# Kernel tuning notes

Hardware: AMD Instinct MI355X
Metric: run time of the kernel (lower is better)

The kernel has to match this reference:

```python
import jax, jax.numpy as jnp
import numpy as np

B, T, F = 256, 288, 64
UNITS = [128, 64, 64, 32]
SCALE = 0.05  # small init so relu-activated recurrence stays numerically stable


def _lstm_scan(x_tbf, Wk, Wr, b):
    """Keras LSTM with activation=relu, recurrent_activation=sigmoid.
    x_tbf: [T, B, in]. Returns all hidden states [T, B, u].
    Gate order in the fused kernel is (i, f, g, o), as in Keras."""
    u = Wr.shape[0]
    bsz = x_tbf.shape[1]

    def step(carry, xt):
        h, c = carry
        z = xt @ Wk + h @ Wr + b            # [B, 4u]
        i, f, g, o = jnp.split(z, 4, axis=-1)
        i = jax.nn.sigmoid(i)
        f = jax.nn.sigmoid(f)
        g = jax.nn.relu(g)                   # cell-input activation = relu
        o = jax.nn.sigmoid(o)
        c = f * c + i * g
        h = o * jax.nn.relu(c)               # output activation = relu
        return (h, c), h

    init = (jnp.zeros((bsz, u), x_tbf.dtype), jnp.zeros((bsz, u), x_tbf.dtype))
    _, hs = jax.lax.scan(step, init, x_tbf)
    return hs  # [T, B, u]


def setup_inputs() -> dict:
    key = jax.random.key(0)
    ks = jax.random.split(key, 20)
    out = {"x": jax.random.normal(ks[0], (B, T, F), dtype=jnp.float32)}
    ins = [F] + UNITS[:-1]
    ki = 1
    for li, (din, u) in enumerate(zip(ins, UNITS), start=1):
        out[f"W{li}"] = jax.random.normal(ks[ki], (din, 4 * u), jnp.float32) * SCALE; ki += 1
        out[f"U{li}"] = jax.random.normal(ks[ki], (u, 4 * u), jnp.float32) * SCALE; ki += 1
        out[f"b{li}"] = jnp.zeros((4 * u,), jnp.float32)
    out["Wf"] = jax.random.normal(ks[ki], (UNITS[-1], 16), jnp.float32) * SCALE; ki += 1
    out["bf"] = jnp.zeros((16,), jnp.float32)
    out["Wo"] = jax.random.normal(ks[ki], (16, 1), jnp.float32) * SCALE
    out["bo"] = jnp.zeros((1,), jnp.float32)
    return out


def reference(x, W1, U1, b1, W2, U2, b2, W3, U3, b3, W4, U4, b4, Wf, bf, Wo, bo):
    # Dropout layers are identity at inference (Keras deterministic call).
    h = jnp.transpose(x, (1, 0, 2))          # [T, B, F] time-major for scan
    h = _lstm_scan(h, W1, U1, b1)            # [T, B, 128]
    h = _lstm_scan(h, W2, U2, b2)            # [T, B, 64]
    h = _lstm_scan(h, W3, U3, b3)            # [T, B, 64]
    h_last = _lstm_scan(h, W4, U4, b4)[-1]   # [B, 32] (return_sequences=False)
    fc = jax.nn.relu(h_last @ Wf + bf)       # [B, 16]
    return fc @ Wo + bo                      # [B, 1]
```

## Files before the change

kernel.cpp:

```cpp
#include <hip/hip_runtime.h>
#include <math.h>

#define TSTEPS 288
#define NTHREADS 512

__device__ __forceinline__ float sigmoidf_(float x) {
    return 1.0f / (1.0f + __expf(-x));
}

template<int NS>
__device__ __forceinline__ float allreduce_seg(float v) {
    if constexpr (NS > 1)
        v += __int_as_float(__builtin_amdgcn_update_dpp(
                0, __float_as_int(v), 0xB1, 0xF, 0xF, true));
    if constexpr (NS > 2)
        v += __int_as_float(__builtin_amdgcn_update_dpp(
                0, __float_as_int(v), 0x4E, 0xF, 0xF, true));
    if constexpr (NS > 4)
        v += __int_as_float(__builtin_amdgcn_ds_swizzle(
                __float_as_int(v), 0x101F));
    return v;
}

template<int DIN, int U, int NS, int ACTIVE, bool FIRST, bool WRITE_NOW, bool WRITE_DELAY>
__device__ void run_layer(const float* __restrict__ Wk,
                          const float* __restrict__ Wr,
                          const float* __restrict__ bias,
                          const float* __restrict__ xg,
                          float* __restrict__ seq,
                          float* __restrict__ xh,
                          float* __restrict__ xring,
                          int tid)
{
    constexpr int KIN  = DIN / NS;
    constexpr int KH   = U / NS;
    constexpr int KT   = KIN + KH;
    constexpr int COLS = 4 * U;
    constexpr int S    = (NS == 4) ? 2 : 3;
    static_assert(ACTIVE == NS * U, "thread mapping");
    static_assert(KIN % 4 == 0 && KH % 4 == 0, "float4 alignment");
    static_assert(NS <= 8, "butterfly width");

    const int seg = tid & (NS - 1);
    const int u   = tid >> S;
    const bool act = tid < ACTIVE;

    float w[4][KT];
    float bz[4] = {0.f, 0.f, 0.f, 0.f};
    float cst = 0.0f, hprev = 0.0f;

    if (act) {
#pragma unroll
        for (int k = 0; k < KIN; ++k) {
            const float* row = Wk + (size_t)(seg * KIN + k) * COLS + u;
#pragma unroll
            for (int g = 0; g < 4; ++g) w[g][k] = row[g * U];
        }
#pragma unroll
        for (int k = 0; k < KH; ++k) {
            const float* row = Wr + (size_t)(seg * KH + k) * COLS + u;
#pragma unroll
            for (int g = 0; g < 4; ++g) w[g][KIN + k] = row[g * U];
        }
        if (seg == 0) {
#pragma unroll
            for (int g = 0; g < 4; ++g) bz[g] = bias[g * U + u];
        }
#pragma unroll
        for (int g = 0; g < 4; ++g)
#pragma unroll
            for (int k = 0; k < KT; ++k)
                asm volatile("" : "+v"(w[g][k]));
    }
    if (tid < 128) xh[tid] = 0.0f;
    if (FIRST && tid < 64) xring[tid] = xg[tid];
    __syncthreads();

    for (int t = 0; t < TSTEPS; ++t) {
        if (act) {
            const float* __restrict__ xr = xh + (t & 1) * 128;
            float* __restrict__ xw       = xh + ((t + 1) & 1) * 128;

            float xstage = 0.0f;
            if (FIRST && tid < 64 && (t + 1) < TSTEPS)
                xstage = xg[(t + 1) * 64 + tid];

            float a0 = bz[0], a1 = bz[1], a2 = bz[2], a3 = bz[3];

            {
                const float* inp = FIRST ? (xring + (t & 1) * 64 + seg * KIN)
                                         : (seq + t * 128 + seg * KIN);
                const float4* in4 = reinterpret_cast<const float4*>(inp);
#pragma unroll
                for (int k4 = 0; k4 < KIN / 4; ++k4) {
                    const float4 v = in4[k4];
                    a0 = fmaf(v.x, w[0][4*k4+0], a0); a1 = fmaf(v.x, w[1][4*k4+0], a1);
                    a2 = fmaf(v.x, w[2][4*k4+0], a2); a3 = fmaf(v.x, w[3][4*k4+0], a3);
                    a0 = fmaf(v.y, w[0][4*k4+1], a0); a1 = fmaf(v.y, w[1][4*k4+1], a1);
                    a2 = fmaf(v.y, w[2][4*k4+1], a2); a3 = fmaf(v.y, w[3][4*k4+1], a3);
                    a0 = fmaf(v.z, w[0][4*k4+2], a0); a1 = fmaf(v.z, w[1][4*k4+2], a1);
                    a2 = fmaf(v.z, w[2][4*k4+2], a2); a3 = fmaf(v.z, w[3][4*k4+2], a3);
                    a0 = fmaf(v.w, w[0][4*k4+3], a0); a1 = fmaf(v.w, w[1][4*k4+3], a1);
                    a2 = fmaf(v.w, w[2][4*k4+3], a2); a3 = fmaf(v.w, w[3][4*k4+3], a3);
                }
            }

            {
                const float4* h4 = reinterpret_cast<const float4*>(xr + seg * KH);
#pragma unroll
                for (int k4 = 0; k4 < KH / 4; ++k4) {
                    const float4 v = h4[k4];
                    const int kb = KIN + 4 * k4;
                    a0 = fmaf(v.x, w[0][kb+0], a0); a1 = fmaf(v.x, w[1][kb+0], a1);
                    a2 = fmaf(v.x, w[2][kb+0], a2); a3 = fmaf(v.x, w[3][kb+0], a3);
                    a0 = fmaf(v.y, w[0][kb+1], a0); a1 = fmaf(v.y, w[1][kb+1], a1);
                    a2 = fmaf(v.y, w[2][kb+1], a2); a3 = fmaf(v.y, w[3][kb+1], a3);
                    a0 = fmaf(v.z, w[0][kb+2], a0); a1 = fmaf(v.z, w[1][kb+2], a1);
                    a2 = fmaf(v.z, w[2][kb+2], a2); a3 = fmaf(v.z, w[3][kb+2], a3);
                    a0 = fmaf(v.w, w[0][kb+3], a0); a1 = fmaf(v.w, w[1][kb+3], a1);
                    a2 = fmaf(v.w, w[2][kb+3], a2); a3 = fmaf(v.w, w[3][kb+3], a3);
                }
            }

            a0 = allreduce_seg<NS>(a0);
            a1 = allreduce_seg<NS>(a1);
            a2 = allreduce_seg<NS>(a2);
            a3 = allreduce_seg<NS>(a3);

            if constexpr (WRITE_DELAY) {
                if (seg == 0 && t > 0) seq[(t - 1) * 128 + u] = hprev;
            }

            const float gi = sigmoidf_(a0);
            const float gf = sigmoidf_(a1);
            const float gg = fmaxf(a2, 0.0f);
            const float go = sigmoidf_(a3);
            cst = fmaf(gf, cst, gi * gg);
            const float h = go * fmaxf(cst, 0.0f);

            if (seg == 0) {
                xw[u] = h;
                if constexpr (WRITE_NOW) seq[t * 128 + u] = h;
            }
            hprev = h;

            if (FIRST && tid < 64 && (t + 1) < TSTEPS)
                xring[((t + 1) & 1) * 64 + tid] = xstage;
        }
        __syncthreads();
    }

    if constexpr (WRITE_DELAY) {
        if (act && seg == 0) seq[(TSTEPS - 1) * 128 + u] = hprev;
    }
}

extern "C" __global__ void __launch_bounds__(NTHREADS, 2)
lstm_stack_kernel(const float* __restrict__ x,
                  const float* __restrict__ W1, const float* __restrict__ U1, const float* __restrict__ b1,
                  const float* __restrict__ W2, const float* __restrict__ U2, const float* __restrict__ b2,
                  const float* __restrict__ W3, const float* __restrict__ U3, const float* __restrict__ b3,
                  const float* __restrict__ W4, const float* __restrict__ U4, const float* __restrict__ b4,
                  const float* __restrict__ Wf, const float* __restrict__ bf,
                  const float* __restrict__ Wo, const float* __restrict__ bo,
                  float* __restrict__ out)
{
    __shared__ __align__(16) float seq[TSTEPS * 128];
    __shared__ __align__(16) float xh[256 + 16];
    __shared__ __align__(16) float xring[2 * 64];

    const int tid = threadIdx.x;
    const float* xg = x + (size_t)blockIdx.x * TSTEPS * 64;

    run_layer< 64, 128, 4, 512, true , true , false>(W1, U1, b1, xg, seq, xh, xring, tid);
    __syncthreads();
    run_layer<128,  64, 8, 512, false, false, true >(W2, U2, b2, xg, seq, xh, xring, tid);
    __syncthreads();
    run_layer< 64,  64, 8, 512, false, false, true >(W3, U3, b3, xg, seq, xh, xring, tid);
    __syncthreads();
    run_layer< 64,  32, 8, 256, false, false, false>(W4, U4, b4, xg, seq, xh, xring, tid);
    __syncthreads();

    if (tid < 16) {
        float acc = bf[tid];
#pragma unroll
        for (int k = 0; k < 32; ++k) acc = fmaf(xh[k], Wf[k * 16 + tid], acc);
        xh[256 + tid] = fmaxf(acc, 0.0f);
    }
    __syncthreads();
    if (tid == 0) {
        float acc = bo[0];
#pragma unroll
        for (int k = 0; k < 16; ++k) acc = fmaf(xh[256 + k], Wo[k], acc);
        out[blockIdx.x] = acc;
    }
}

extern "C" void kernel_launch(void* const* d_in, const int* in_sizes, int n_in,
                              void* d_out, int out_size, void* d_ws, size_t ws_size,
                              hipStream_t stream) {
    const float* x  = (const float*)d_in[0];
    const float* W1 = (const float*)d_in[1];
    const float* U1 = (const float*)d_in[2];
    const float* b1 = (const float*)d_in[3];
    const float* W2 = (const float*)d_in[4];
    const float* U2 = (const float*)d_in[5];
    const float* b2 = (const float*)d_in[6];
    const float* W3 = (const float*)d_in[7];
    const float* U3 = (const float*)d_in[8];
    const float* b3 = (const float*)d_in[9];
    const float* W4 = (const float*)d_in[10];
    const float* U4 = (const float*)d_in[11];
    const float* b4 = (const float*)d_in[12];
    const float* Wf = (const float*)d_in[13];
    const float* bf = (const float*)d_in[14];
    const float* Wo = (const float*)d_in[15];
    const float* bo = (const float*)d_in[16];
    float* out = (float*)d_out;

    lstm_stack_kernel<<<dim3(256), dim3(NTHREADS), 0, stream>>>(
        x, W1, U1, b1, W2, U2, b2, W3, U3, b3, W4, U4, b4, Wf, bf, Wo, bo, out);
}
```

Baseline: 699.3 us.

## Use packed FP32 FMA and interleave shared-memory vectors to avoid bank conflicts

Weights are now held as float2 pairs and the gate dot products use v_pk_fma_f32, which halves the FMA instruction count per step. The hidden-state and sequence buffers in shared memory are written in a permuted order, so that each segment's float4 reads are strided across segments instead of contiguous, which is meant to reduce LDS bank conflicts. This adds a horizontal add of the two packed lanes and relies on the permutation layouts of producer and consumer layers matching.

```diff
diff --git a/kernel.cpp b/kernel.cpp
--- a/kernel.cpp
+++ b/kernel.cpp
@@ -4,8 +4,14 @@
 #define TSTEPS 288
 #define NTHREADS 512
 
+typedef float f32x2 __attribute__((ext_vector_type(2)));
+
 __device__ __forceinline__ float sigmoidf_(float x) {
     return 1.0f / (1.0f + __expf(-x));
+}
+
+__device__ __forceinline__ void pkfma(f32x2& acc, f32x2 w, f32x2 x) {
+    asm("v_pk_fma_f32 %0, %1, %2, %0" : "+v"(acc) : "v"(w), "v"(x));
 }
 
 template<int NS>
@@ -22,7 +28,13 @@
     return v;
 }
 
-template<int DIN, int U, int NS, int ACTIVE, bool FIRST, bool WRITE_NOW, bool WRITE_DELAY>
+template<int NS, int KSEG>
+__device__ __forceinline__ int perm_idx(int j) {
+    return (((j % KSEG) >> 2) * NS + (j / KSEG)) * 4 + (j & 3);
+}
+
+template<int DIN, int U, int NS, int ACTIVE, int SEQNS, int SEQK,
+         bool FIRST, bool WRITE_NOW, bool WRITE_DELAY>
 __device__ void run_layer(const float* __restrict__ Wk,
                           const float* __restrict__ Wr,
                           const float* __restrict__ bias,
@@ -34,33 +46,42 @@
 {
     constexpr int KIN  = DIN / NS;
     constexpr int KH   = U / NS;
-    constexpr int KT   = KIN + KH;
     constexpr int COLS = 4 * U;
     constexpr int S    = (NS == 4) ? 2 : 3;
+    constexpr int NPI  = KIN / 2;
+    constexpr int NPH  = KH / 2;
     static_assert(ACTIVE == NS * U, "thread mapping");
-    static_assert(KIN % 4 == 0 && KH % 4 == 0, "float4 alignment");
+    static_assert(KIN % 4 == 0 && (KH % 4 == 0), "float4 alignment");
     static_assert(NS <= 8, "butterfly width");
 
     const int seg = tid & (NS - 1);
     const int u   = tid >> S;
     const bool act = tid < ACTIVE;
 
-    float w[4][KT];
+    f32x2 w[4][NPI + NPH];
     float bz[4] = {0.f, 0.f, 0.f, 0.f};
     float cst = 0.0f, hprev = 0.0f;
 
     if (act) {
 #pragma unroll
-        for (int k = 0; k < KIN; ++k) {
-            const float* row = Wk + (size_t)(seg * KIN + k) * COLS + u;
-#pragma unroll
-            for (int g = 0; g < 4; ++g) w[g][k] = row[g * U];
-        }
-#pragma unroll
-        for (int k = 0; k < KH; ++k) {
-            const float* row = Wr + (size_t)(seg * KH + k) * COLS + u;
-#pragma unroll
-            for (int g = 0; g < 4; ++g) w[g][KIN + k] = row[g * U];
+        for (int p = 0; p < NPI; ++p) {
+            const int k0 = seg * KIN + 2 * p;
+#pragma unroll
+            for (int g = 0; g < 4; ++g) {
+                const int c = g * U + u;
+                w[g][p] = f32x2{Wk[(size_t)k0 * COLS + c],
+                                Wk[(size_t)(k0 + 1) * COLS + c]};
+            }
+        }
+#pragma unroll
+        for (int p = 0; p < NPH; ++p) {
+            const int k0 = seg * KH + 2 * p;
+#pragma unroll
+            for (int g = 0; g < 4; ++g) {
+                const int c = g * U + u;
+                w[g][NPI + p] = f32x2{Wr[(size_t)k0 * COLS + c],
+                                      Wr[(size_t)(k0 + 1) * COLS + c]};
+            }
         }
         if (seg == 0) {
 #pragma unroll
@@ -69,11 +90,12 @@
 #pragma unroll
         for (int g = 0; g < 4; ++g)
 #pragma unroll
-            for (int k = 0; k < KT; ++k)
-                asm volatile("" : "+v"(w[g][k]));
+            for (int p = 0; p < NPI + NPH; ++p)
+                asm volatile("" : "+v"(w[g][p]));
     }
     if (tid < 128) xh[tid] = 0.0f;
-    if (FIRST && tid < 64) xring[tid] = xg[tid];
+    if (FIRST && tid < 64)
+        xring[perm_idx<4, 16>(tid)] = xg[tid];
     __syncthreads();
 
     for (int t = 0; t < TSTEPS; ++t) {
@@ -85,50 +107,48 @@
             if (FIRST && tid < 64 && (t + 1) < TSTEPS)
                 xstage = xg[(t + 1) * 64 + tid];
 
-            float a0 = bz[0], a1 = bz[1], a2 = bz[2], a3 = bz[3];
+            f32x2 ac0 = {0.f, 0.f}, ac1 = {0.f, 0.f},
+                  ac2 = {0.f, 0.f}, ac3 = {0.f, 0.f};
 
             {
-                const float* inp = FIRST ? (xring + (t & 1) * 64 + seg * KIN)
-                                         : (seq + t * 128 + seg * KIN);
-                const float4* in4 = reinterpret_cast<const float4*>(inp);
+                const float4* in4 = reinterpret_cast<const float4*>(
+                    FIRST ? (xring + (t & 1) * 64) : (seq + t * 128)) + seg;
 #pragma unroll
                 for (int k4 = 0; k4 < KIN / 4; ++k4) {
-                    const float4 v = in4[k4];
-                    a0 = fmaf(v.x, w[0][4*k4+0], a0); a1 = fmaf(v.x, w[1][4*k4+0], a1);
-                    a2 = fmaf(v.x, w[2][4*k4+0], a2); a3 = fmaf(v.x, w[3][4*k4+0], a3);
-                    a0 = fmaf(v.y, w[0][4*k4+1], a0); a1 = fmaf(v.y, w[1][4*k4+1], a1);
-                    a2 = fmaf(v.y, w[2][4*k4+1], a2); a3 = fmaf(v.y, w[3][4*k4+1], a3);
-                    a0 = fmaf(v.z, w[0][4*k4+2], a0); a1 = fmaf(v.z, w[1][4*k4+2], a1);
-                    a2 = fmaf(v.z, w[2][4*k4+2], a2); a3 = fmaf(v.z, w[3][4*k4+2], a3);
-                    a0 = fmaf(v.w, w[0][4*k4+3], a0); a1 = fmaf(v.w, w[1][4*k4+3], a1);
-                    a2 = fmaf(v.w, w[2][4*k4+3], a2); a3 = fmaf(v.w, w[3][4*k4+3], a3);
+                    const float4 v = in4[k4 * NS];
+                    const f32x2 lo = {v.x, v.y}, hi = {v.z, v.w};
+                    pkfma(ac0, w[0][2*k4+0], lo); pkfma(ac0, w[0][2*k4+1], hi);
+                    pkfma(ac1, w[1][2*k4+0], lo); pkfma(ac1, w[1][2*k4+1], hi);
+                    pkfma(ac2, w[2][2*k4+0], lo); pkfma(ac2, w[2][2*k4+1], hi);
+                    pkfma(ac3, w[3][2*k4+0], lo); pkfma(ac3, w[3][2*k4+1], hi);
                 }
             }
-
             {
-                const float4* h4 = reinterpret_cast<const float4*>(xr + seg * KH);
+                const float4* h4 = reinterpret_cast<const float4*>(xr) + seg;
 #pragma unroll
                 for (int k4 = 0; k4 < KH / 4; ++k4) {
-                    const float4 v = h4[k4];
-                    const int kb = KIN + 4 * k4;
-                    a0 = fmaf(v.x, w[0][kb+0], a0); a1 = fmaf(v.x, w[1][kb+0], a1);
-                    a2 = fmaf(v.x, w[2][kb+0], a2); a3 = fmaf(v.x, w[3][kb+0], a3);
-                    a0 = fmaf(v.y, w[0][kb+1], a0); a1 = fmaf(v.y, w[1][kb+1], a1);
-                    a2 = fmaf(v.y, w[2][kb+1], a2); a3 = fmaf(v.y, w[3][kb+1], a3);
-                    a0 = fmaf(v.z, w[0][kb+2], a0); a1 = fmaf(v.z, w[1][kb+2], a1);
-                    a2 = fmaf(v.z, w[2][kb+2], a2); a3 = fmaf(v.z, w[3][kb+2], a3);
-                    a0 = fmaf(v.w, w[0][kb+3], a0); a1 = fmaf(v.w, w[1][kb+3], a1);
-                    a2 = fmaf(v.w, w[2][kb+3], a2); a3 = fmaf(v.w, w[3][kb+3], a3);
+                    const float4 v = h4[k4 * NS];
+                    const f32x2 lo = {v.x, v.y}, hi = {v.z, v.w};
+                    const int pb = NPI + 2 * k4;
+                    pkfma(ac0, w[0][pb], lo); pkfma(ac0, w[0][pb+1], hi);
+                    pkfma(ac1, w[1][pb], lo); pkfma(ac1, w[1][pb+1], hi);
+                    pkfma(ac2, w[2][pb], lo); pkfma(ac2, w[2][pb+1], hi);
+                    pkfma(ac3, w[3][pb], lo); pkfma(ac3, w[3][pb+1], hi);
                 }
             }
 
+            float a0 = (ac0[0] + ac0[1]) + bz[0];
+            float a1 = (ac1[0] + ac1[1]) + bz[1];
+            float a2 = (ac2[0] + ac2[1]) + bz[2];
+            float a3 = (ac3[0] + ac3[1]) + bz[3];
             a0 = allreduce_seg<NS>(a0);
             a1 = allreduce_seg<NS>(a1);
             a2 = allreduce_seg<NS>(a2);
             a3 = allreduce_seg<NS>(a3);
 
             if constexpr (WRITE_DELAY) {
-                if (seg == 0 && t > 0) seq[(t - 1) * 128 + u] = hprev;
+                if (seg == 0 && t > 0)
+                    seq[(t - 1) * 128 + perm_idx<SEQNS, SEQK>(u)] = hprev;
             }
 
             const float gi = sigmoidf_(a0);
@@ -139,19 +159,21 @@
             const float h = go * fmaxf(cst, 0.0f);
 
             if (seg == 0) {
-                xw[u] = h;
-                if constexpr (WRITE_NOW) seq[t * 128 + u] = h;
+                xw[perm_idx<NS, KH>(u)] = h;
+                if constexpr (WRITE_NOW)
+                    seq[t * 128 + perm_idx<SEQNS, SEQK>(u)] = h;
             }
             hprev = h;
 
             if (FIRST && tid < 64 && (t + 1) < TSTEPS)
-                xring[((t + 1) & 1) * 64 + tid] = xstage;
+                xring[((t + 1) & 1) * 64 + perm_idx<4, 16>(tid)] = xstage;
         }
         __syncthreads();
     }
 
     if constexpr (WRITE_DELAY) {
-        if (act && seg == 0) seq[(TSTEPS - 1) * 128 + u] = hprev;
+        if (act && seg == 0)
+            seq[(TSTEPS - 1) * 128 + perm_idx<SEQNS, SEQK>(u)] = hprev;
     }
 }
 
@@ -172,13 +194,13 @@
     const int tid = threadIdx.x;
     const float* xg = x + (size_t)blockIdx.x * TSTEPS * 64;
 
-    run_layer< 64, 128, 4, 512, true , true , false>(W1, U1, b1, xg, seq, xh, xring, tid);
-    __syncthreads();
-    run_layer<128,  64, 8, 512, false, false, true >(W2, U2, b2, xg, seq, xh, xring, tid);
-    __syncthreads();
-    run_layer< 64,  64, 8, 512, false, false, true >(W3, U3, b3, xg, seq, xh, xring, tid);
-    __syncthreads();
-    run_layer< 64,  32, 8, 256, false, false, false>(W4, U4, b4, xg, seq, xh, xring, tid);
+    run_layer< 64, 128, 4, 512,  8, 16, true , true , false>(W1, U1, b1, xg, seq, xh, xring, tid);
+    __syncthreads();
+    run_layer<128,  64, 8, 512,  8,  8, false, false, true >(W2, U2, b2, xg, seq, xh, xring, tid);
+    __syncthreads();
+    run_layer< 64,  64, 8, 512,  8,  8, false, false, true >(W3, U3, b3, xg, seq, xh, xring, tid);
+    __syncthreads();
+    run_layer< 64,  32, 8, 256,  8,  8, false, false, false>(W4, U4, b4, xg, seq, xh, xring, tid);
     __syncthreads();
 
     if (tid < 16) {
```

Result: slower. 713.5 us (+2.0%).
